# Kernel tuning notes

Measured on AMD Instinct MI355X. Metric: run time of the kernel, lower is better.

## Reference

```python
import jax, jax.numpy as jnp
import numpy as np

BALL_SIZE = 128


def setup_inputs() -> dict:
    key = jax.random.key(0)
    kq, kk, kv = jax.random.split(key, 3)
    B, H, n, Dh = 4, 16, 8192, 64
    q = jax.random.normal(kq, (B, H, n, Dh), dtype=jnp.float32)
    k = jax.random.normal(kk, (B, H, n, Dh), dtype=jnp.float32)
    v = jax.random.normal(kv, (B, H, n, Dh), dtype=jnp.float32)
    return {"q": q, "k": k, "v": v}


def reference(q, k, v) -> jnp.ndarray:
    # Block-local (ball) attention: attention computed independently within
    # each contiguous ball of size BALL_SIZE along the sequence dim.
    B, H, n, Dh = q.shape
    bs = BALL_SIZE
    m = n // bs
    # (B, H, m, bs, D) -- split seq into balls; attention only within a ball.
    qb = q.reshape(B, H, m, bs, Dh)
    kb = k.reshape(B, H, m, bs, Dh)
    vb = v.reshape(B, H, m, bs, Dh)
    scale = 1.0 / jnp.sqrt(jnp.asarray(Dh, dtype=q.dtype))
    scores = jnp.einsum('bhmqd,bhmkd->bhmqk', qb, kb) * scale  # (B,H,m,bs,bs)
    attn = jax.nn.softmax(scores, axis=-1)
    out = jnp.einsum('bhmqk,bhmkd->bhmqd', attn, vb)
    return out.reshape(B, H, n, Dh)
```

## Files before the change

### kernel.cpp

```cpp
#include <hip/hip_runtime.h>

typedef _Float16 half2_t __attribute__((ext_vector_type(2)));
typedef _Float16 half4_t __attribute__((ext_vector_type(4)));
typedef _Float16 half8_t __attribute__((ext_vector_type(8)));
typedef __fp16   fp16x2  __attribute__((ext_vector_type(2)));
typedef float    f32x4   __attribute__((ext_vector_type(4)));

#define BS 128
#define DH 64

__device__ __forceinline__ half2_t pkrtz(float x, float y) {
  fp16x2 t = __builtin_amdgcn_cvt_pkrtz(x, y);
  return __builtin_bit_cast(half2_t, t);
}

__device__ __forceinline__ half8_t cvt8(const float4 a, const float4 b) {
  half2_t h0 = pkrtz(a.x, a.y);
  half2_t h1 = pkrtz(a.z, a.w);
  half2_t h2 = pkrtz(b.x, b.y);
  half2_t h3 = pkrtz(b.z, b.w);
  half4_t lo = __builtin_shufflevector(h0, h1, 0, 1, 2, 3);
  half4_t hi = __builtin_shufflevector(h2, h3, 0, 1, 2, 3);
  return __builtin_shufflevector(lo, hi, 0, 1, 2, 3, 4, 5, 6, 7);
}

__device__ __forceinline__ int svt(int d) { return (d & 7) ^ ((d >> 2) & 7); }

__global__ __launch_bounds__(256) void ball_attn_kernel(
    const float* __restrict__ Q, const float* __restrict__ Kk,
    const float* __restrict__ V, float* __restrict__ O) {
  __shared__ __align__(16) _Float16 VT[DH * BS];
  __shared__ __align__(16) _Float16 Pl[4 * 16 * BS];

  const int tid  = threadIdx.x;
  const int w    = tid >> 6;
  const int lane = tid & 63;
  const int c    = lane & 15;
  const int g    = lane >> 4;

  const int nwg  = gridDim.x;
  const int bid  = blockIdx.x;
  const int ball = (bid & 7) * (nwg >> 3) + (bid >> 3);

  const size_t base = (size_t)ball * (BS * DH);
  const float* Qb = Q + base;
  const float* Kb = Kk + base;
  const float* Vb = V + base;
  float*       Ob = O + base;

  {
    const int kgrp = tid >> 4;
    const int d0   = (tid & 15) * 4;
    float4 vA[4], vB[4];
#pragma unroll
    for (int it = 0; it < 4; ++it) {
      const int keyA = 2 * kgrp + 32 * it;
      vA[it] = *(const float4*)(Vb + (size_t)keyA * DH + d0);
      vB[it] = *(const float4*)(Vb + (size_t)(keyA + 1) * DH + d0);
    }
#pragma unroll
    for (int it = 0; it < 4; ++it) {
      const int keyA = 2 * kgrp + 32 * it;
      const float* ap = (const float*)&vA[it];
      const float* bp = (const float*)&vB[it];
#pragma unroll
      for (int j = 0; j < 4; ++j) {
        const int d = d0 + j;
        *(half2_t*)&VT[d * BS + (keyA ^ (svt(d) << 3))] = pkrtz(ap[j], bp[j]);
      }
    }
  }

  half8_t aq[2][2];
#pragma unroll
  for (int m = 0; m < 2; ++m)
#pragma unroll
    for (int ks = 0; ks < 2; ++ks) {
      const float* qp = Qb + (w * 32 + m * 16 + c) * DH + ks * 32 + g * 8;
      aq[m][ks] = cvt8(*(const float4*)qp, *(const float4*)(qp + 4));
    }

  __syncthreads();

  f32x4 acc[2][8];
#pragma unroll
  for (int m = 0; m < 2; ++m)
#pragma unroll
    for (int kt = 0; kt < 8; ++kt) acc[m][kt] = (f32x4){0.f, 0.f, 0.f, 0.f};

  {
    float4 kb[2][2];
    auto kaddr = [&](int i) {
      const int kt = i >> 1, ks = i & 1;
      return Kb + (kt * 16 + c) * DH + ks * 32 + g * 8;
    };
    kb[0][0] = *(const float4*)kaddr(0);
    kb[0][1] = *(const float4*)(kaddr(0) + 4);
    kb[1][0] = *(const float4*)kaddr(1);
    kb[1][1] = *(const float4*)(kaddr(1) + 4);
#pragma unroll
    for (int i = 0; i < 16; ++i) {
      const half8_t bk = cvt8(kb[i & 1][0], kb[i & 1][1]);
      if (i + 2 < 16) {
        kb[i & 1][0] = *(const float4*)kaddr(i + 2);
        kb[i & 1][1] = *(const float4*)(kaddr(i + 2) + 4);
      }
      const int kt = i >> 1, ks = i & 1;
      acc[0][kt] = __builtin_amdgcn_mfma_f32_16x16x32_f16(aq[0][ks], bk, acc[0][kt], 0, 0, 0);
      acc[1][kt] = __builtin_amdgcn_mfma_f32_16x16x32_f16(aq[1][ks], bk, acc[1][kt], 0, 0, 0);
    }
  }

#pragma unroll
  for (int m = 0; m < 2; ++m) {
    float mx[4], sm[4], inv[4];
#pragma unroll
    for (int r = 0; r < 4; ++r) {
      mx[r] = acc[m][0][r];
#pragma unroll
      for (int kt = 1; kt < 8; ++kt) mx[r] = fmaxf(mx[r], acc[m][kt][r]);
    }
#pragma unroll
    for (int r = 0; r < 4; ++r) {
      mx[r] = fmaxf(mx[r], __shfl_xor(mx[r], 1));
      mx[r] = fmaxf(mx[r], __shfl_xor(mx[r], 2));
      mx[r] = fmaxf(mx[r], __shfl_xor(mx[r], 4));
      mx[r] = fmaxf(mx[r], __shfl_xor(mx[r], 8));
      sm[r] = 0.f;
    }
#pragma unroll
    for (int kt = 0; kt < 8; ++kt)
#pragma unroll
      for (int r = 0; r < 4; ++r) {
        const float p = __expf((acc[m][kt][r] - mx[r]) * 0.125f);
        acc[m][kt][r] = p;
        sm[r] += p;
      }
#pragma unroll
    for (int r = 0; r < 4; ++r) {
      sm[r] += __shfl_xor(sm[r], 1);
      sm[r] += __shfl_xor(sm[r], 2);
      sm[r] += __shfl_xor(sm[r], 4);
      sm[r] += __shfl_xor(sm[r], 8);
      inv[r] = __builtin_amdgcn_rcpf(sm[r]);
    }
#pragma unroll
    for (int kt = 0; kt < 8; ++kt)
#pragma unroll
      for (int r = 0; r < 4; ++r) {
        const int row = 4 * g + r;
        Pl[(w * 16 + row) * BS + ((kt * 16 + c) ^ ((row & 7) << 3))] =
            (_Float16)acc[m][kt][r];
      }

    f32x4 o[4];
#pragma unroll
    for (int t = 0; t < 4; ++t) o[t] = (f32x4){0.f, 0.f, 0.f, 0.f};
#pragma unroll
    for (int ks = 0; ks < 4; ++ks) {
      const int e0 = ks * 32 + g * 8;
      const half8_t pfg = *(const half8_t*)&Pl[(w * 16 + c) * BS + (e0 ^ ((c & 7) << 3))];
#pragma unroll
      for (int t = 0; t < 4; ++t) {
        const int rowd = t * 16 + c;
        const half8_t vf = *(const half8_t*)&VT[rowd * BS + (e0 ^ (svt(rowd) << 3))];
        o[t] = __builtin_amdgcn_mfma_f32_16x16x32_f16(pfg, vf, o[t], 0, 0, 0);
      }
    }
#pragma unroll
    for (int t = 0; t < 4; ++t)
#pragma unroll
      for (int r = 0; r < 4; ++r)
        Ob[(w * 32 + m * 16 + 4 * g + r) * DH + t * 16 + c] = o[t][r] * inv[r];
  }
}

extern "C" void kernel_launch(void* const* d_in, const int* in_sizes, int n_in,
                              void* d_out, int out_size, void* d_ws, size_t ws_size,
                              hipStream_t stream) {
  const float* q = (const float*)d_in[0];
  const float* k = (const float*)d_in[1];
  const float* v = (const float*)d_in[2];
  float* out = (float*)d_out;
  const int nballs = in_sizes[0] / (BS * DH);
  ball_attn_kernel<<<dim3(nballs), dim3(256), 0, stream>>>(q, k, v, out);
}
```

Before: 131.6 us.

## Stage K through LDS via async global_load_lds and use nontemporal output stores

```diff
diff --git a/kernel.cpp b/kernel.cpp
--- a/kernel.cpp
+++ b/kernel.cpp
@@ -29,6 +29,7 @@
 __global__ __launch_bounds__(256) void ball_attn_kernel(
     const float* __restrict__ Q, const float* __restrict__ Kk,
     const float* __restrict__ V, float* __restrict__ O) {
+  __shared__ __align__(16) float    Kf[BS * DH];
   __shared__ __align__(16) _Float16 VT[DH * BS];
   __shared__ __align__(16) _Float16 Pl[4 * 16 * BS];
 
@@ -48,6 +49,17 @@
   const float* Vb = V + base;
   float*       Ob = O + base;
 
+#pragma unroll
+  for (int t = 0; t < 8; ++t) {
+    const int row = 32 * w + 4 * t + g;
+    const int u   = c ^ (row & 7);
+    __builtin_amdgcn_global_load_lds(
+        (const __attribute__((address_space(1))) unsigned int*)(Kb + row * DH + u * 4),
+        (__attribute__((address_space(3))) unsigned int*)&Kf[(32 * w + 4 * t) * DH],
+        16, 0, 0);
+  }
+
+  half8_t aq[2][2];
   {
     const int kgrp = tid >> 4;
     const int d0   = (tid & 15) * 4;
@@ -58,6 +70,13 @@
       vA[it] = *(const float4*)(Vb + (size_t)keyA * DH + d0);
       vB[it] = *(const float4*)(Vb + (size_t)(keyA + 1) * DH + d0);
     }
+#pragma unroll
+    for (int m = 0; m < 2; ++m)
+#pragma unroll
+      for (int ks = 0; ks < 2; ++ks) {
+        const float* qp = Qb + (w * 32 + m * 16 + c) * DH + ks * 32 + g * 8;
+        aq[m][ks] = cvt8(*(const float4*)qp, *(const float4*)(qp + 4));
+      }
 #pragma unroll
     for (int it = 0; it < 4; ++it) {
       const int keyA = 2 * kgrp + 32 * it;
@@ -71,15 +90,6 @@
     }
   }
 
-  half8_t aq[2][2];
-#pragma unroll
-  for (int m = 0; m < 2; ++m)
-#pragma unroll
-    for (int ks = 0; ks < 2; ++ks) {
-      const float* qp = Qb + (w * 32 + m * 16 + c) * DH + ks * 32 + g * 8;
-      aq[m][ks] = cvt8(*(const float4*)qp, *(const float4*)(qp + 4));
-    }
-
   __syncthreads();
 
   f32x4 acc[2][8];
@@ -88,28 +98,19 @@
 #pragma unroll
     for (int kt = 0; kt < 8; ++kt) acc[m][kt] = (f32x4){0.f, 0.f, 0.f, 0.f};
 
-  {
-    float4 kb[2][2];
-    auto kaddr = [&](int i) {
-      const int kt = i >> 1, ks = i & 1;
-      return Kb + (kt * 16 + c) * DH + ks * 32 + g * 8;
-    };
-    kb[0][0] = *(const float4*)kaddr(0);
-    kb[0][1] = *(const float4*)(kaddr(0) + 4);
-    kb[1][0] = *(const float4*)kaddr(1);
-    kb[1][1] = *(const float4*)(kaddr(1) + 4);
 #pragma unroll
-    for (int i = 0; i < 16; ++i) {
-      const half8_t bk = cvt8(kb[i & 1][0], kb[i & 1][1]);
-      if (i + 2 < 16) {
-        kb[i & 1][0] = *(const float4*)kaddr(i + 2);
-        kb[i & 1][1] = *(const float4*)(kaddr(i + 2) + 4);
-      }
-      const int kt = i >> 1, ks = i & 1;
+  for (int kt = 0; kt < 8; ++kt)
+#pragma unroll
+    for (int ks = 0; ks < 2; ++ks) {
+      const int row = kt * 16 + c;
+      const int sr  = row & 7;
+      const int u0  = 8 * ks + 2 * g;
+      const float4 a = *(const float4*)&Kf[row * DH + ((u0 ^ sr) * 4)];
+      const float4 b = *(const float4*)&Kf[row * DH + (((u0 + 1) ^ sr) * 4)];
+      const half8_t bk = cvt8(a, b);
       acc[0][kt] = __builtin_amdgcn_mfma_f32_16x16x32_f16(aq[0][ks], bk, acc[0][kt], 0, 0, 0);
       acc[1][kt] = __builtin_amdgcn_mfma_f32_16x16x32_f16(aq[1][ks], bk, acc[1][kt], 0, 0, 0);
     }
-  }
 
 #pragma unroll
   for (int m = 0; m < 2; ++m) {
@@ -171,7 +172,8 @@
     for (int t = 0; t < 4; ++t)
 #pragma unroll
       for (int r = 0; r < 4; ++r)
-        Ob[(w * 32 + m * 16 + 4 * g + r) * DH + t * 16 + c] = o[t][r] * inv[r];
+        __builtin_nontemporal_store(
+            o[t][r] * inv[r], &Ob[(w * 32 + m * 16 + 4 * g + r) * DH + t * 16 + c]);
   }
 }
 
```

After: 121.8 us. 1.08x faster.
